# Kernel optimization log

Measured on AMD Instinct MI355X. Metric: run time of the kernel, lower is better.

## Reference

```python
import jax, jax.numpy as jnp
import numpy as np

jax.config.update("jax_enable_x64", True)  # original solves the quartic in double/complex128

MU = 1.33
SCALE = 1.0
N_RAYS = 2_000_000


def _solve2nd(a, b, c):
    # roots of a x^2 + b x + c, complex128
    D = (b * b - 4 * a * c).astype(jnp.complex128)
    s = jnp.sqrt(D)
    return (-b + s) / (2 * a), (-b - s) / (2 * a)


def _solve3rd(a, b, c, d):
    # Cardano closed form, returns [N,3] complex128
    A0 = d / a
    A1 = c / a
    A2 = b / a
    p = A1 - A2 * A2 / 3
    q = A0 - A1 * A2 / 3 + A2 * A2 * A2 * 2 / 27
    D = (q / 2) ** 2 + (p / 3) ** 3 + 1e-12
    r = jnp.sqrt(D.astype(jnp.complex128))
    o = complex(-0.5, np.sqrt(3) / 2)
    L = jnp.power(-q / 2 + r, 1.0 / 3.0)
    R = jnp.power(-q / 2 - r, 1.0 / 3.0)
    x0 = L + R - A2 / 3
    x1 = o * o * L + o * R - A2 / 3
    x2 = o * L + o * o * R - A2 / 3
    return jnp.stack([x0, x1, x2], axis=-1)


def _solve4th(coefs):
    # Ferrari via resolvent cubic; coefs [N,5] float64 -> roots [N,4] complex128
    a, b, c, d, e = (coefs[..., i] for i in range(5))
    A0 = e / a
    A1 = d / a
    A2 = c / a
    A3 = b / a
    p = A2 - 6 * A3 * A3 / 16
    q = A1 - A2 * A3 / 2 + 8 * (A3 / 4) ** 3
    r = A0 - A1 * A3 / 4 + A2 * A3 * A3 / 16 - 3 * (A3 / 4) ** 4
    u = _solve3rd(jnp.ones_like(p), 2 * p, p * p - 4 * r, -q * q)  # [N,3] complex
    cost = jnp.where(u.real < 0, 1e6, jnp.abs(u.imag))
    idx = jnp.argmin(cost, axis=1)
    t = jnp.clip(jnp.take_along_axis(u.real, idx[:, None], axis=1)[:, 0], 1e-6, None)
    st = jnp.sqrt(t)
    y00, y01 = _solve2nd(jnp.ones_like(t), st, (p + t) / 2 - st * q / (2 * t))
    y10, y11 = _solve2nd(jnp.ones_like(t), -st, (p + t) / 2 + st * q / (2 * t))
    return jnp.stack([y00 - A3 / 4, y01 - A3 / 4, y10 - A3 / 4, y11 - A3 / 4], axis=-1)


def _forward_projection(pos3d, n, d_eff, mu):
    nvec = jnp.concatenate([n, jnp.ones((1,), pos3d.dtype)])
    normal = -(nvec / jnp.linalg.norm(nvec))[None, :]          # [1,3]
    por = jnp.cross(normal, pos3d)                              # [N,3]
    por = por / jnp.linalg.norm(por, axis=-1, keepdims=True)
    z1 = -normal                                                # [1,3]
    z2 = jnp.cross(por, jnp.broadcast_to(z1, por.shape))        # [N,3]
    v = jnp.sum(pos3d * z1, axis=-1)                            # [N]
    u = jnp.sum(pos3d * z2, axis=-1)                            # [N]
    c2 = -2 * u * (mu - 1) * (mu + 1)
    c1 = jnp.ones_like(c2) * ((mu - 1) * (mu + 1))
    c3 = d_eff * d_eff * mu * mu - d_eff * d_eff + 2 * d_eff * v + mu * mu * u * u - u * u - v * v
    c4 = -2 * d_eff * d_eff * mu * mu * u
    c5 = d_eff * d_eff * mu * mu * u * u
    coefs = jnp.stack([c1, c2, c3, c4, c5], axis=-1).astype(jnp.float64)
    x0 = _solve4th(coefs).astype(jnp.complex64).T               # [4,N]
    xx = x0.real.astype(jnp.float32)                            # [4,N]
    n2 = jnp.array([0.0, -1.0], jnp.float32)
    vi = jnp.stack([xx, jnp.ones_like(xx) * d_eff], axis=-1)    # [4,N,2]
    bb = jnp.sum(vi * n2, axis=-1)
    bbb = jnp.sum(vi * vi, axis=-1)
    b = (-bb - jnp.sqrt(bb * bb - (1 - mu * mu) * bbb)) / mu
    vr = (1.0 / mu) * vi + b[..., None] * n2                    # refracted 2D dirs
    vrd = jnp.stack([u, v], axis=-1)[None] - vi                 # [4,N,2]
    error = jnp.abs(vrd[..., 0] * vr[..., 1] - vrd[..., 1] * vr[..., 0])
    error = jnp.where(jnp.abs(x0.imag) > 0.001, jnp.inf, error)
    best = jnp.take_along_axis(xx, jnp.argmin(error, axis=0)[None, :], axis=0)[0]
    return best[:, None] * z2 + d_eff * z1                      # [N,3]


def setup_inputs() -> dict:
    key = jax.random.key(0)
    k1, k2, k3 = jax.random.split(key, 3)
    pos3d = jax.random.normal(k1, (N_RAYS, 3), dtype=jnp.float32)
    # put points at positive depth so refraction geometry is sensible
    pos3d = pos3d.at[:, 2].set(jnp.abs(pos3d[:, 2]) + 0.5)
    n = jax.random.normal(k2, (2,), dtype=jnp.float32) * 0.02   # near-flat interface normal xy
    d = jax.random.uniform(k3, (), dtype=jnp.float32) * 0.5 + 0.2  # scalar depth param
    return {"pos3d": pos3d, "n": n, "d": d}


def reference(pos3d, n, d):
    mu = jnp.float32(MU)
    d_eff = jax.nn.relu(d) / SCALE + 0.001
    return _forward_projection(pos3d, n, d_eff, mu)
```

## Files before the change

### kernel.cpp

```cpp
#include <hip/hip_runtime.h>
#include <math.h>


__device__ __forceinline__ double cbrt_fast(double x) {
    if (x < 1e-30) return 0.0;
    double w = (double)(1.0f / cbrtf((float)x));
    w = w * (4.0 - x * ((w * w) * w)) * (1.0 / 3.0);
    return x * (w * w);
}

__global__ __launch_bounds__(256) void refract_kernel(
    const float* __restrict__ pos,
    const float* __restrict__ nrm,
    const float* __restrict__ dpt,
    float* __restrict__ out,
    int N)
{
    int i = blockIdx.x * blockDim.x + threadIdx.x;
    if (i >= N) return;

    const float mu = 1.33f;
    float n0 = nrm[0], n1 = nrm[1];
    float d_eff = fmaxf(dpt[0], 0.0f) + 0.001f;

    float nn = sqrtf(n0 * n0 + n1 * n1 + 1.0f);
    float z1x = n0 / nn, z1y = n1 / nn, z1z = 1.0f / nn;

    float px = pos[3 * i + 0], py = pos[3 * i + 1], pz = pos[3 * i + 2];

    float cux = z1y * pz - z1z * py;
    float cuy = z1z * px - z1x * pz;
    float cuz = z1x * py - z1y * px;
    float pn = sqrtf(cux * cux + cuy * cuy + cuz * cuz);
    float u = -pn;
    float ipn = 1.0f / pn;
    float z2x = (z1y * cuz - z1z * cuy) * ipn;
    float z2y = (z1z * cux - z1x * cuz) * ipn;
    float z2z = (z1x * cuy - z1y * cux) * ipn;

    float v = px * z1x + py * z1y + pz * z1z;

    float c2f = -2.0f * u * (mu - 1.0f) * (mu + 1.0f);
    float c3f = d_eff * d_eff * mu * mu - d_eff * d_eff + 2.0f * d_eff * v
              + mu * mu * u * u - u * u - v * v;
    float c4f = -2.0f * d_eff * d_eff * mu * mu * u;
    float c5f = d_eff * d_eff * mu * mu * u * u;

    const double invc1 = 1.0 / (double)((1.33f - 1.0f) * (1.33f + 1.0f));
    double A0 = (double)c5f * invc1;
    double A1 = (double)c4f * invc1;
    double A2 = (double)c3f * invc1;
    double A3 = (double)c2f * invc1;

    double h = A3 * 0.25;
    double p = A2 - (6.0 * A3) * A3 * 0.0625;
    double q = A1 - A2 * A3 * 0.5 + 8.0 * ((h * h) * h);
    double r = A0 - A1 * A3 * 0.25 + ((A2 * A3) * A3) * 0.0625
             - 3.0 * ((h * h) * (h * h));

    double B2 = 2.0 * p;
    double B1 = p * p - 4.0 * r;
    double B0 = -(q * q);
    double pc  = B1 - B2 * B2 * (1.0 / 3.0);
    double qc  = B0 - B1 * B2 * (1.0 / 3.0) + ((B2 * B2) * B2) * (2.0 / 27.0);
    double hq  = qc * 0.5;
    double pc3 = pc * (1.0 / 3.0);
    double Dc  = hq * hq + (pc3 * pc3) * pc3 + 1e-12;
    double mql = -hq;
    double sh  = B2 * (1.0 / 3.0);

    double t;
    bool polish;

    if (Dc < 0.0) {
        float rr  = sqrtf((float)(-pc3));
        float rho = rr * rr * rr;
        float cphi = fminf(fmaxf((float)mql / rho, -1.0f), 1.0f);
        float yy = 2.0f * rr * cosf(acosf(cphi) * (1.0f / 3.0f));
        t = (double)yy - sh;
        polish = true;
    } else {
        double rcr;
        if (Dc < 1e-24) {
            rcr = 0.0;
        } else {
            double z = (double)rsqrtf((float)Dc);
            z = z * (1.5 - 0.5 * Dc * (z * z));
            rcr = Dc * z;
        }
        double aa = mql + rcr;
        double bb = mql - rcr;
        if (aa >= 0.0 && bb >= 0.0) {
            t = (double)(cbrtf((float)aa) + cbrtf((float)bb)) - sh;
            polish = true;
        } else {
            double ya = cbrt_fast(fabs(aa));
            double yb = cbrt_fast(fabs(bb));
            const double CI = 0.8660254037844386;
            double Lre, Lim, Rre, Rim;
            if (aa >= 0.0) { Lre = ya;       Lim = 0.0;     }
            else           { Lre = 0.5 * ya; Lim = CI * ya; }
            if (bb >= 0.0) { Rre = yb;       Rim = 0.0;     }
            else           { Rre = 0.5 * yb; Rim = CI * yb; }
            const double o_re = -0.5, o_im = CI;
            const double o2_re = o_re * o_re - o_im * o_im;
            const double o2_im = 2.0 * o_re * o_im;
            double u0r = Lre + Rre - sh;
            double u0i = Lim + Rim;
            double u1r = (o2_re * Lre - o2_im * Lim) + (o_re * Rre - o_im * Rim) - sh;
            double u1i = (o2_re * Lim + o2_im * Lre) + (o_re * Rim + o_im * Rre);
            double u2r = (o_re * Lre - o_im * Lim) + (o2_re * Rre - o2_im * Rim) - sh;
            double u2i = (o_re * Lim + o_im * Lre) + (o2_re * Rim + o2_im * Rre);
            double cost0 = (u0r < 0.0) ? 1e6 : fabs(u0i);
            double cost1 = (u1r < 0.0) ? 1e6 : fabs(u1i);
            double cost2 = (u2r < 0.0) ? 1e6 : fabs(u2i);
            t = u0r; double cbv = cost0;
            if (cost1 < cbv) { cbv = cost1; t = u1r; }
            if (cost2 < cbv) { cbv = cost2; t = u2r; }
            polish = false;
        }
    }

    if (polish) {
        double f   = ((t + B2) * t + B1) * t + B0;
        double fp  = (3.0 * t + 2.0 * B2) * t + B1;
        double fpp = 6.0 * t + 2.0 * B2;
        double den = fp * fp - 0.5 * f * fpp;
        double inv = (double)(1.0f / (float)den);
        inv = inv * (2.0 - den * inv);
        double dt  = (f * fp) * inv;
        if (isfinite(dt) && fabs(dt) < 0.1 * fabs(t) + 1e-2) t -= dt;
    }

    t = fmax(t, 1e-6);
    double rs = (double)rsqrtf((float)t);
    rs = rs * (1.5 - 0.5 * t * (rs * rs));
    double st = t * rs;
    double w  = (q * rs) * 0.5;
    double pt2 = (p + t) * 0.5;
    double stst = st * st;
    double D1 = stst - 4.0 * (pt2 - w);
    double D2 = stst - 4.0 * (pt2 + w);

    float s1r = 0.0f, s1i = 0.0f, s2r = 0.0f, s2i = 0.0f;
    if (D1 >= 0.0) s1r = sqrtf((float)D1); else s1i = sqrtf((float)(-D1));
    if (D2 >= 0.0) s2r = sqrtf((float)D2); else s2i = sqrtf((float)(-D2));
    bool im1 = (s1i * 0.5f > 0.001f);
    bool im2 = (s2i * 0.5f > 0.001f);

    float stf = (float)st;
    float hf  = (float)h;
    float xr0 = (-stf + s1r) * 0.5f - hf;
    float xr1 = (-stf - s1r) * 0.5f - hf;
    float xr2 = ( stf + s2r) * 0.5f - hf;
    float xr3 = ( stf - s2r) * 0.5f - hf;

    float mm2 = mu * mu - 1.0f;
    float mude2 = mu * mu * d_eff * d_eff;
    float vd = v - d_eff;
    float e0, e1, e2, e3;
    {
        float g;
        g = fmaf(mm2, xr0 * xr0, mude2);
        e0 = im1 ? INFINITY : fabsf((u - xr0) * sqrtf(g) - vd * xr0);
        g = fmaf(mm2, xr1 * xr1, mude2);
        e1 = im1 ? INFINITY : fabsf((u - xr1) * sqrtf(g) - vd * xr1);
        g = fmaf(mm2, xr2 * xr2, mude2);
        e2 = im2 ? INFINITY : fabsf((u - xr2) * sqrtf(g) - vd * xr2);
        g = fmaf(mm2, xr3 * xr3, mude2);
        e3 = im2 ? INFINITY : fabsf((u - xr3) * sqrtf(g) - vd * xr3);
    }
    float best = xr0; float eb = e0;
    if (e1 < eb) { eb = e1; best = xr1; }
    if (e2 < eb) { eb = e2; best = xr2; }
    if (e3 < eb) { eb = e3; best = xr3; }

    out[3 * i + 0] = best * z2x + d_eff * z1x;
    out[3 * i + 1] = best * z2y + d_eff * z1y;
    out[3 * i + 2] = best * z2z + d_eff * z1z;
}

extern "C" void kernel_launch(void* const* d_in, const int* in_sizes, int n_in,
                              void* d_out, int out_size, void* d_ws, size_t ws_size,
                              hipStream_t stream) {
    const float* pos = (const float*)d_in[0];
    const float* nrm = (const float*)d_in[1];
    const float* dpt = (const float*)d_in[2];
    float* out = (float*)d_out;
    int N = in_sizes[0] / 3;
    int block = 256;
    int grid = (N + block - 1) / block;
    refract_kernel<<<grid, block, 0, stream>>>(pos, nrm, dpt, out, N);
}
```

Measured before the change: 32.37 us.

## Replace transcendentals with hardware intrinsics and branch-free cubic root selection

```diff
diff --git a/kernel.cpp b/kernel.cpp
--- a/kernel.cpp
+++ b/kernel.cpp
@@ -2,11 +2,17 @@
 #include <math.h>
 
 
-__device__ __forceinline__ double cbrt_fast(double x) {
-    if (x < 1e-30) return 0.0;
-    double w = (double)(1.0f / cbrtf((float)x));
+__device__ __forceinline__ float fast_rcp(float x) { return __builtin_amdgcn_rcpf(x); }
+__device__ __forceinline__ float fast_rsq(float x) { return __builtin_amdgcn_rsqf(x); }
+
+__device__ __forceinline__ double cbrt2(double x) {
+    float xf = (float)x;
+    float wf = __builtin_amdgcn_exp2f(__builtin_amdgcn_logf(xf) * (-1.0f / 3.0f));
+    double w = (double)wf;
     w = w * (4.0 - x * ((w * w) * w)) * (1.0 / 3.0);
-    return x * (w * w);
+    w = w * (4.0 - x * ((w * w) * w)) * (1.0 / 3.0);
+    double c = x * (w * w);
+    return (x < 1e-30) ? 0.0 : c;
 }
 
 __global__ __launch_bounds__(256) void refract_kernel(
@@ -33,7 +39,7 @@
     float cuz = z1x * py - z1y * px;
     float pn = sqrtf(cux * cux + cuy * cuy + cuz * cuz);
     float u = -pn;
-    float ipn = 1.0f / pn;
+    float ipn = fast_rcp(pn);
     float z2x = (z1y * cuz - z1z * cuy) * ipn;
     float z2y = (z1z * cux - z1x * cuz) * ipn;
     float z2z = (z1x * cuy - z1y * cux) * ipn;
@@ -73,52 +79,54 @@
     bool polish;
 
     if (Dc < 0.0) {
-        float rr  = sqrtf((float)(-pc3));
-        float rho = rr * rr * rr;
-        float cphi = fminf(fmaxf((float)mql / rho, -1.0f), 1.0f);
-        float yy = 2.0f * rr * cosf(acosf(cphi) * (1.0f / 3.0f));
-        t = (double)yy - sh;
+        float R2f = (float)(-pc3);
+        float Rf  = sqrtf(R2f);
+        float cphi = (float)mql * fast_rcp(R2f * Rf);
+        cphi = fminf(fmaxf(cphi, -1.0f), 1.0f);
+        float T = 0.5f + sqrtf((1.0f + cphi) * (1.0f / 6.0f));
+        #pragma unroll
+        for (int k = 0; k < 3; ++k) {
+            float g  = fmaf(fmaf(4.0f * T, T, -3.0f), T, -cphi);
+            float gp = fmaf(12.0f * T, T, -3.0f);
+            T -= g * fast_rcp(gp + 1e-12f);
+        }
+        t = (double)(2.0f * Rf * T) - sh;
         polish = true;
     } else {
         double rcr;
-        if (Dc < 1e-24) {
+        if (Dc < 1e-36) {
             rcr = 0.0;
         } else {
-            double z = (double)rsqrtf((float)Dc);
+            double z = (double)fast_rsq((float)Dc);
             z = z * (1.5 - 0.5 * Dc * (z * z));
             rcr = Dc * z;
         }
         double aa = mql + rcr;
         double bb = mql - rcr;
-        if (aa >= 0.0 && bb >= 0.0) {
-            t = (double)(cbrtf((float)aa) + cbrtf((float)bb)) - sh;
-            polish = true;
-        } else {
-            double ya = cbrt_fast(fabs(aa));
-            double yb = cbrt_fast(fabs(bb));
-            const double CI = 0.8660254037844386;
-            double Lre, Lim, Rre, Rim;
-            if (aa >= 0.0) { Lre = ya;       Lim = 0.0;     }
-            else           { Lre = 0.5 * ya; Lim = CI * ya; }
-            if (bb >= 0.0) { Rre = yb;       Rim = 0.0;     }
-            else           { Rre = 0.5 * yb; Rim = CI * yb; }
-            const double o_re = -0.5, o_im = CI;
-            const double o2_re = o_re * o_re - o_im * o_im;
-            const double o2_im = 2.0 * o_re * o_im;
-            double u0r = Lre + Rre - sh;
-            double u0i = Lim + Rim;
-            double u1r = (o2_re * Lre - o2_im * Lim) + (o_re * Rre - o_im * Rim) - sh;
-            double u1i = (o2_re * Lim + o2_im * Lre) + (o_re * Rim + o_im * Rre);
-            double u2r = (o_re * Lre - o_im * Lim) + (o2_re * Rre - o2_im * Rim) - sh;
-            double u2i = (o_re * Lim + o_im * Lre) + (o2_re * Rim + o2_im * Rre);
-            double cost0 = (u0r < 0.0) ? 1e6 : fabs(u0i);
-            double cost1 = (u1r < 0.0) ? 1e6 : fabs(u1i);
-            double cost2 = (u2r < 0.0) ? 1e6 : fabs(u2i);
-            t = u0r; double cbv = cost0;
-            if (cost1 < cbv) { cbv = cost1; t = u1r; }
-            if (cost2 < cbv) { cbv = cost2; t = u2r; }
-            polish = false;
-        }
+        bool na = (aa < 0.0), nb = (bb < 0.0);
+        double ca = cbrt2(fabs(aa));
+        double cb = cbrt2(fabs(bb));
+
+        const double CI = 0.8660254037844386;
+        double Lre = na ? 0.5 * ca : ca;
+        double Lim = na ? CI * ca  : 0.0;
+        double Rre = nb ? 0.5 * cb : cb;
+        double Rim = nb ? CI * cb  : 0.0;
+
+        double u0r = (Lre + Rre) - sh;
+        double u0i =  Lim + Rim;
+        double u1r = (-0.5 * Lre + CI * Lim) + (-0.5 * Rre - CI * Rim) - sh;
+        double u1i = (-0.5 * Lim - CI * Lre) + (-0.5 * Rim + CI * Rre);
+        double u2r = (-0.5 * Lre - CI * Lim) + (-0.5 * Rre + CI * Rim) - sh;
+        double u2i = (-0.5 * Lim + CI * Lre) + (-0.5 * Rim - CI * Rre);
+
+        double c0 = (u0r < 0.0) ? 1e6 : fabs(u0i);
+        double c1 = (u1r < 0.0) ? 1e6 : fabs(u1i);
+        double c2 = (u2r < 0.0) ? 1e6 : fabs(u2i);
+        int bi = 0; double cbest = c0; t = u0r;
+        if (c1 < cbest) { cbest = c1; t = u1r; bi = 1; }
+        if (c2 < cbest) { cbest = c2; t = u2r; bi = 2; }
+        polish = (!na && !nb && bi == 0);
     }
 
     if (polish) {
@@ -126,14 +134,14 @@
         double fp  = (3.0 * t + 2.0 * B2) * t + B1;
         double fpp = 6.0 * t + 2.0 * B2;
         double den = fp * fp - 0.5 * f * fpp;
-        double inv = (double)(1.0f / (float)den);
+        double inv = (double)fast_rcp((float)den);
         inv = inv * (2.0 - den * inv);
         double dt  = (f * fp) * inv;
         if (isfinite(dt) && fabs(dt) < 0.1 * fabs(t) + 1e-2) t -= dt;
     }
 
     t = fmax(t, 1e-6);
-    double rs = (double)rsqrtf((float)t);
+    double rs = (double)fast_rsq((float)t);
     rs = rs * (1.5 - 0.5 * t * (rs * rs));
     double st = t * rs;
     double w  = (q * rs) * 0.5;
@@ -158,18 +166,15 @@
     float mm2 = mu * mu - 1.0f;
     float mude2 = mu * mu * d_eff * d_eff;
     float vd = v - d_eff;
-    float e0, e1, e2, e3;
-    {
-        float g;
-        g = fmaf(mm2, xr0 * xr0, mude2);
-        e0 = im1 ? INFINITY : fabsf((u - xr0) * sqrtf(g) - vd * xr0);
-        g = fmaf(mm2, xr1 * xr1, mude2);
-        e1 = im1 ? INFINITY : fabsf((u - xr1) * sqrtf(g) - vd * xr1);
-        g = fmaf(mm2, xr2 * xr2, mude2);
-        e2 = im2 ? INFINITY : fabsf((u - xr2) * sqrtf(g) - vd * xr2);
-        g = fmaf(mm2, xr3 * xr3, mude2);
-        e3 = im2 ? INFINITY : fabsf((u - xr3) * sqrtf(g) - vd * xr3);
-    }
+    float g0 = fmaf(mm2, xr0 * xr0, mude2);
+    float g1 = fmaf(mm2, xr1 * xr1, mude2);
+    float g2 = fmaf(mm2, xr2 * xr2, mude2);
+    float g3 = fmaf(mm2, xr3 * xr3, mude2);
+    float e0 = im1 ? INFINITY : fabsf((u - xr0) * sqrtf(g0) - vd * xr0);
+    float e1 = im1 ? INFINITY : fabsf((u - xr1) * sqrtf(g1) - vd * xr1);
+    float e2 = im2 ? INFINITY : fabsf((u - xr2) * sqrtf(g2) - vd * xr2);
+    float e3 = im2 ? INFINITY : fabsf((u - xr3) * sqrtf(g3) - vd * xr3);
+
     float best = xr0; float eb = e0;
     if (e1 < eb) { eb = e1; best = xr1; }
     if (e2 < eb) { eb = e2; best = xr2; }
```

Measured after the change: 32.24 us. No clear change (-0.4%).
